# Optimization experiments

Hardware: AMD Instinct MI355X
Metric: run time of the kernel (lower is better)

## Reference

```python
import jax, jax.numpy as jnp
import numpy as np

B, T, C, H = 4, 2048, 768, 12
D = C // H  # head dim = 64
EPS = 1e-5


def setup_inputs() -> dict:
    key = jax.random.key(0)
    ks = jax.random.split(key, 12)
    s = lambda fan_in: 1.0 / np.sqrt(fan_in)
    return {
        "x": jax.random.normal(ks[0], (B, T, C), dtype=jnp.float32),
        "ln1_g": jnp.ones((C,), jnp.float32),
        "ln1_b": jnp.zeros((C,), jnp.float32),
        "w_attn": jax.random.normal(ks[1], (C, 3 * C), jnp.float32) * s(C),
        "b_attn": jnp.zeros((3 * C,), jnp.float32),
        "w_aproj": jax.random.normal(ks[2], (C, C), jnp.float32) * s(C),
        "b_aproj": jnp.zeros((C,), jnp.float32),
        "ln2_g": jnp.ones((C,), jnp.float32),
        "ln2_b": jnp.zeros((C,), jnp.float32),
        "w_fc": jax.random.normal(ks[3], (C, 4 * C), jnp.float32) * s(C),
        "b_fc": jnp.zeros((4 * C,), jnp.float32),
        "w_mproj": jax.random.normal(ks[4], (4 * C, C), jnp.float32) * s(4 * C),
        "b_mproj": jnp.zeros((C,), jnp.float32),
    }


def _layernorm(x, g, b):
    mu = jnp.mean(x, axis=-1, keepdims=True)
    var = jnp.mean(jnp.square(x - mu), axis=-1, keepdims=True)
    return (x - mu) * jax.lax.rsqrt(var + EPS) * g + b


def _attention(h, w_attn, b_attn, w_aproj, b_aproj):
    qkv = h @ w_attn + b_attn                          # [B,T,3C]
    q, k, v = jnp.split(qkv, 3, axis=-1)
    q = q.reshape(B, T, H, D)
    k = k.reshape(B, T, H, D)
    v = v.reshape(B, T, H, D)
    att = jnp.einsum("bqhd,bkhd->bhqk", q, k) * (1.0 / np.sqrt(D))
    causal = jnp.tril(jnp.ones((T, T), bool))
    att = jnp.where(causal, att, -jnp.inf)
    att = jax.nn.softmax(att, axis=-1)
    y = jnp.einsum("bhqk,bkhd->bqhd", att, v).reshape(B, T, C)
    return y @ w_aproj + b_aproj


def reference(x, ln1_g, ln1_b, w_attn, b_attn, w_aproj, b_aproj,
              ln2_g, ln2_b, w_fc, b_fc, w_mproj, b_mproj):
    x = x + _attention(_layernorm(x, ln1_g, ln1_b), w_attn, b_attn, w_aproj, b_aproj)
    h = _layernorm(x, ln2_g, ln2_b)
    h = jax.nn.gelu(h @ w_fc + b_fc, approximate=True)  # tanh approximation, matches F.gelu(approximate='tanh')
    x = x + (h @ w_mproj + b_mproj)
    return x
```

## Files before the change

### kernel.cpp

```cpp
#include <hip/hip_runtime.h>


typedef unsigned short ushortT;
typedef unsigned int uintT;
typedef __attribute__((ext_vector_type(8))) __bf16 bf16x8;
typedef __attribute__((ext_vector_type(4))) float f32x4;

#define MFMA16(a, b, c) __builtin_amdgcn_mfma_f32_16x16x32_bf16(a, b, c, 0, 0, 0)

__device__ inline float b2f(ushortT u) {
  return __uint_as_float(((uintT)u) << 16);
}
__device__ inline ushortT f2b(float f) {
  uintT x = __float_as_uint(f);
  uintT r = x + 0x7fffu + ((x >> 16) & 1u);
  return (ushortT)(r >> 16);
}
__device__ inline uintT pack_bf2(float a, float b) {
  return __builtin_amdgcn_perm(__float_as_uint(b), __float_as_uint(a),
                               0x07060302u);
}

__device__ inline float gelu_tanh(float v) {
  float t = 0.7978845608028654f * (v + 0.044715f * v * v * v);
  return v / (1.0f + __expf(-2.0f * t));
}

__device__ __forceinline__ void glds16(const ushortT* g, ushortT* l) {
  __builtin_amdgcn_global_load_lds(
      (const __attribute__((address_space(1))) unsigned int*)(const void*)g,
      (__attribute__((address_space(3))) unsigned int*)(void*)l, 16, 0, 0);
}

__global__ __launch_bounds__(256) void detect_dtype(
    const ushortT* __restrict__ w, int* __restrict__ flag) {
  __shared__ int red;
  if (threadIdx.x == 0) red = 0;
  __syncthreads();
  int crazy = 0;
  for (int i = threadIdx.x; i < 4096; i += 256) {
    uintT e = (w[2 * i] >> 7) & 0xFF;
    if (e >= 150) crazy = 1;
  }
  if (crazy) atomicOr(&red, 1);
  __syncthreads();
  if (threadIdx.x == 0) *flag = red;
}

struct VecArgs {
  const void* src[8];
  int n[8];
  int dstoff[8];
};
__global__ __launch_bounds__(256) void convert_vecs(
    VecArgs a, ushortT* __restrict__ pv, const int* __restrict__ flag) {
  int fl = *flag;
  int t = blockIdx.y;
  int i = blockIdx.x * 256 + threadIdx.x;
  if (i >= a.n[t]) return;
  float v = fl ? ((const float*)a.src[t])[i] : b2f(((const ushortT*)a.src[t])[i]);
  pv[a.dstoff[t] + i] = f2b(v);
}

__global__ __launch_bounds__(256) void transpose_any(
    const void* __restrict__ in, ushortT* __restrict__ out, int K, int N,
    const int* __restrict__ flag) {
  __shared__ ushortT t[32][33];
  int fl = *flag;
  int n0 = blockIdx.x * 32, k0 = blockIdx.y * 32;
  int x = threadIdx.x, y0 = threadIdx.y;
#pragma unroll
  for (int i = y0; i < 32; i += 8) {
    size_t idx = (size_t)(k0 + i) * N + n0 + x;
    t[i][x] = fl ? f2b(((const float*)in)[idx]) : ((const ushortT*)in)[idx];
  }
  __syncthreads();
#pragma unroll
  for (int i = y0; i < 32; i += 8)
    out[(size_t)(n0 + i) * K + k0 + x] = t[x][i];
}

__global__ __launch_bounds__(256) void vtrans_kernel(
    const ushortT* __restrict__ qkv, ushortT* __restrict__ vt) {
  const int T = 2048, C3 = 2304;
  __shared__ ushortT tile[64][65];
  int bh = blockIdx.y;
  int b = bh / 12, h = bh % 12;
  int t0 = blockIdx.x * 64;
  int col = threadIdx.x & 63, rowi = threadIdx.x >> 6;
#pragma unroll
  for (int rr = rowi; rr < 64; rr += 4)
    tile[rr][col] =
        qkv[((size_t)(b * T + t0 + rr)) * C3 + 1536 + h * 64 + col];
  __syncthreads();
#pragma unroll
  for (int dd = rowi; dd < 64; dd += 4)
    vt[((size_t)bh * 64 + dd) * T + t0 + col] = tile[col][dd];
}

template <int MODE>
__global__ __launch_bounds__(256) void ln_kernel(
    const void* __restrict__ xin, const ushortT* __restrict__ g,
    const ushortT* __restrict__ bb, ushortT* __restrict__ out,
    const int* __restrict__ flag) {
  const int C = 768;
  bool f32;
  if constexpr (MODE == 1) f32 = true; else f32 = (*flag != 0);
  size_t base = (size_t)blockIdx.x * C;
  int tid = threadIdx.x;
  const float* xf = (const float*)xin;
  const ushortT* xb = (const ushortT*)xin;
  float v0 = f32 ? xf[base + tid]       : b2f(xb[base + tid]);
  float v1 = f32 ? xf[base + tid + 256] : b2f(xb[base + tid + 256]);
  float v2 = f32 ? xf[base + tid + 512] : b2f(xb[base + tid + 512]);
  float s = v0 + v1 + v2;
  float q = v0 * v0 + v1 * v1 + v2 * v2;
#pragma unroll
  for (int off = 32; off; off >>= 1) {
    s += __shfl_xor(s, off);
    q += __shfl_xor(q, off);
  }
  __shared__ float as_[4], aq_[4];
  if ((tid & 63) == 0) { as_[tid >> 6] = s; aq_[tid >> 6] = q; }
  __syncthreads();
  s = as_[0] + as_[1] + as_[2] + as_[3];
  q = aq_[0] + aq_[1] + aq_[2] + aq_[3];
  float mu = s * (1.0f / 768.0f);
  float var = q * (1.0f / 768.0f) - mu * mu;
  float rs = rsqrtf(var + 1e-5f);
  ushortT* orow = out + base;
  orow[tid]       = f2b((v0 - mu) * rs * b2f(g[tid])       + b2f(bb[tid]));
  orow[tid + 256] = f2b((v1 - mu) * rs * b2f(g[tid + 256]) + b2f(bb[tid + 256]));
  orow[tid + 512] = f2b((v2 - mu) * rs * b2f(g[tid + 512]) + b2f(bb[tid + 512]));
}

template <int EPI, int MT, int BN, int NBN>
__global__ __launch_bounds__(256) void gemm_bf16(
    const ushortT* __restrict__ A, const ushortT* __restrict__ Bt,
    const ushortT* __restrict__ bias, const void* __restrict__ res,
    void* __restrict__ out, int N, int K, int nbm,
    const int* __restrict__ flag) {
  constexpr int MI = MT / 32, NI = BN / 32;
  __shared__ ushortT As[2 * MT * 32];
  __shared__ ushortT Bs[2 * BN * 32];
  int fl = (EPI >= 2) ? *flag : 0;
  int tid = threadIdx.x;
  int lane = tid & 63, wave = tid >> 6;
  int quad = lane >> 4, n = lane & 15;
  int wm = (wave >> 1) * (MT >> 1), wn = (wave & 1) * (BN >> 1);
  int l = blockIdx.x;
  int xcd = l & 7, j = l >> 3;
  int m0 = (xcd * (nbm >> 3) + j / NBN) * MT;
  int n0 = (j % NBN) * BN;

  int srow = lane >> 2, scol = (lane & 3) << 3;
  const ushortT* pa = A + (size_t)(m0 + wave * 16 + srow) * K + scol;
  const ushortT* pb = Bt + (size_t)(n0 + wave * 16 + srow) * K + scol;

  f32x4 acc[MI][NI] = {};

  for (int k0 = 0; k0 < K; k0 += 64) {
    __syncthreads();
#pragma unroll
    for (int i = 0; i < MT / 64; ++i) {
      glds16(pa + (size_t)i * 64 * K + k0, As + (wave * 16 + i * 64) * 32);
      glds16(pa + (size_t)i * 64 * K + k0 + 32,
             As + MT * 32 + (wave * 16 + i * 64) * 32);
    }
#pragma unroll
    for (int i = 0; i < BN / 64; ++i) {
      glds16(pb + (size_t)i * 64 * K + k0, Bs + (wave * 16 + i * 64) * 32);
      glds16(pb + (size_t)i * 64 * K + k0 + 32,
             Bs + BN * 32 + (wave * 16 + i * 64) * 32);
    }
    __syncthreads();
#pragma unroll
    for (int kk = 0; kk < 2; ++kk) {
      const ushortT* ap = As + kk * MT * 32;
      const ushortT* bp = Bs + kk * BN * 32;
      bf16x8 af[MI], bfr[NI];
#pragma unroll
      for (int mi = 0; mi < MI; ++mi)
        af[mi] = *(const bf16x8*)(ap + (wm + mi * 16 + n) * 32 + quad * 8);
#pragma unroll
      for (int ni = 0; ni < NI; ++ni)
        bfr[ni] = *(const bf16x8*)(bp + (wn + ni * 16 + n) * 32 + quad * 8);
#pragma unroll
      for (int mi = 0; mi < MI; ++mi)
#pragma unroll
        for (int ni = 0; ni < NI; ++ni)
          acc[mi][ni] = MFMA16(af[mi], bfr[ni], acc[mi][ni]);
    }
  }

#pragma unroll
  for (int mi = 0; mi < MI; ++mi) {
#pragma unroll
    for (int ni = 0; ni < NI; ++ni) {
      int gc = n0 + wn + ni * 16 + n;
      float bv = b2f(bias[gc]);
      int gr0 = m0 + wm + mi * 16 + quad * 4;
#pragma unroll
      for (int r = 0; r < 4; ++r) {
        size_t idx = (size_t)(gr0 + r) * N + gc;
        float v = acc[mi][ni][r] + bv;
        if constexpr (EPI == 1) v = gelu_tanh(v);
        if constexpr (EPI == 2) {
          v += fl ? ((const float*)res)[idx] : b2f(((const ushortT*)res)[idx]);
          ((float*)out)[idx] = v;
        } else if constexpr (EPI == 3) {
          v += ((const float*)res)[idx];
          if (fl) ((float*)out)[idx] = v;
          else    ((ushortT*)out)[idx] = f2b(v);
        } else {
          ((ushortT*)out)[idx] = f2b(v);
        }
      }
    }
  }
}

__global__ __launch_bounds__(256) void attn_kernel(
    const ushortT* __restrict__ qkv, const ushortT* __restrict__ vt,
    ushortT* __restrict__ y) {
  const int T = 2048, C3 = 2304;
  constexpr int LDK = 72, LDP = 72;
  __shared__ ushortT Ks[64 * LDK];
  __shared__ ushortT Vs[64 * LDK];
  __shared__ ushortT Ps[4 * 16 * LDP];
  int bh = blockIdx.y;
  int b = bh / 12, h = bh % 12;
  int pj = blockIdx.x;
  int tid = threadIdx.x;
  int lane = tid & 63, wave = tid >> 6;
  int quad = lane >> 4, n = lane & 15;

  const ushortT* base = qkv + (size_t)b * T * C3;
  const ushortT* kbase = base + 768 + h * 64;
  const ushortT* vbase = vt + (size_t)bh * 64 * T;
  ushortT* myP = Ps + wave * 16 * LDP;

  const float QS = 0.18033688011112042f;
  const float MB = 20.0f;

  int qtA = pj, qtB = 31 - pj;
  int nA = qtA + 1, ntot = 33;

  int trow = tid >> 3, tcol = (tid & 7) << 3;
  const ushortT* kg = kbase + (size_t)trow * C3 + tcol;
  const ushortT* vg = vbase + (size_t)trow * T + tcol;

  int qt = qtA;
  int qw = qt * 64 + wave * 16;
  bf16x8 aq[2];
  {
    const ushortT* qrow = base + (size_t)(qw + n) * C3 + h * 64 + quad * 8;
#pragma unroll
    for (int dh = 0; dh < 2; ++dh) {
      union { ushortT u[8]; bf16x8 v; } tmp;
#pragma unroll
      for (int j = 0; j < 8; ++j) tmp.u[j] = f2b(b2f(qrow[dh * 32 + j]) * QS);
      aq[dh] = tmp.v;
    }
  }
  f32x4 Ot[4] = {};
  float l_ = 0.f;

  uint4 kr0 = *(const uint4*)(kg);
  uint4 kr1 = *(const uint4*)(kg + (size_t)32 * C3);
  uint4 vr0 = *(const uint4*)(vg);
  uint4 vr1 = *(const uint4*)(vg + (size_t)32 * T);

  for (int t = 0; t < ntot; ++t) {
    int kt = (t < nA) ? t : t - nA;
    __syncthreads();
    *(uint4*)(Ks + trow * LDK + tcol) = kr0;
    *(uint4*)(Ks + (trow + 32) * LDK + tcol) = kr1;
    *(uint4*)(Vs + trow * LDK + tcol) = vr0;
    *(uint4*)(Vs + (trow + 32) * LDK + tcol) = vr1;
    __syncthreads();
    if (t + 1 < ntot) {
      int ktn = (t + 1 < nA) ? t + 1 : t + 1 - nA;
      int k0n = ktn << 6;
      kr0 = *(const uint4*)(kg + (size_t)k0n * C3);
      kr1 = *(const uint4*)(kg + (size_t)(k0n + 32) * C3);
      vr0 = *(const uint4*)(vg + k0n);
      vr1 = *(const uint4*)(vg + (size_t)32 * T + k0n);
    }

    f32x4 St[4];
#pragma unroll
    for (int g = 0; g < 4; ++g) {
      bf16x8 ka0 = *(const bf16x8*)(Ks + (g * 16 + n) * LDK + quad * 8);
      bf16x8 ka1 = *(const bf16x8*)(Ks + (g * 16 + n) * LDK + 32 + quad * 8);
      f32x4 z = {};
      z = MFMA16(ka0, aq[0], z);
      St[g] = MFMA16(ka1, aq[1], z);
    }
    if (kt == qt) {
      int lim = wave * 16 + n;
#pragma unroll
      for (int g = 0; g < 4; ++g)
#pragma unroll
        for (int r = 0; r < 4; ++r)
          if (g * 16 + quad * 4 + r > lim) St[g][r] = -1e30f;
    }
    float ls = 0.f;
#pragma unroll
    for (int g = 0; g < 4; ++g) {
      float p0 = exp2f(St[g][0] - MB);
      float p1 = exp2f(St[g][1] - MB);
      float p2 = exp2f(St[g][2] - MB);
      float p3 = exp2f(St[g][3] - MB);
      ls += (p0 + p1) + (p2 + p3);
      uint2 pk;
      pk.x = pack_bf2(p0, p1);
      pk.y = pack_bf2(p2, p3);
      *(uint2*)(myP + n * LDP + g * 16 + quad * 4) = pk;
    }
    ls += __shfl_xor(ls, 16);
    ls += __shfl_xor(ls, 32);
    l_ += ls;

    bf16x8 pb0 = *(const bf16x8*)(myP + n * LDP + quad * 8);
    bf16x8 pb1 = *(const bf16x8*)(myP + n * LDP + 32 + quad * 8);
#pragma unroll
    for (int dt = 0; dt < 4; ++dt) {
      bf16x8 va0 = *(const bf16x8*)(Vs + (dt * 16 + n) * LDK + quad * 8);
      bf16x8 va1 = *(const bf16x8*)(Vs + (dt * 16 + n) * LDK + 32 + quad * 8);
      Ot[dt] = MFMA16(va0, pb0, Ot[dt]);
      Ot[dt] = MFMA16(va1, pb1, Ot[dt]);
    }

    if (kt == qt) {
      float inv = 1.0f / l_;
      int qg = qw + n;
#pragma unroll
      for (int dt = 0; dt < 4; ++dt) {
        uint2 o;
        o.x = pack_bf2(Ot[dt][0] * inv, Ot[dt][1] * inv);
        o.y = pack_bf2(Ot[dt][2] * inv, Ot[dt][3] * inv);
        *(uint2*)(y + (size_t)(b * T + qg) * 768 + h * 64 + dt * 16 +
                  quad * 4) = o;
      }
      if (t + 1 < ntot) {
        qt = qtB;
        qw = qt * 64 + wave * 16;
        const ushortT* qrow =
            base + (size_t)(qw + n) * C3 + h * 64 + quad * 8;
#pragma unroll
        for (int dh = 0; dh < 2; ++dh) {
          union { ushortT u[8]; bf16x8 v; } tmp;
#pragma unroll
          for (int j = 0; j < 8; ++j)
            tmp.u[j] = f2b(b2f(qrow[dh * 32 + j]) * QS);
          aq[dh] = tmp.v;
        }
#pragma unroll
        for (int dt = 0; dt < 4; ++dt)
#pragma unroll
          for (int r = 0; r < 4; ++r) Ot[dt][r] = 0.f;
        l_ = 0.f;
      }
    }
  }
}

extern "C" void kernel_launch(void* const* d_in, const int* in_sizes, int n_in,
                              void* d_out, int out_size, void* d_ws,
                              size_t ws_size, hipStream_t stream) {
  (void)in_sizes; (void)n_in; (void)out_size; (void)ws_size;
  const void* x       = d_in[0];
  const void* w_attn  = d_in[3];
  const void* w_aproj = d_in[5];
  const void* w_fc    = d_in[9];
  const void* w_mproj = d_in[11];

  char* ws = (char*)d_ws;
  ushortT* h1  = (ushortT*)(ws);
  ushortT* qkv = (ushortT*)(ws + 12582912);
  ushortT* yb  = (ushortT*)(ws + 50331648);
  float*   x1  = (float*)(ws + 62914560);
  ushortT* fcg = (ushortT*)(ws + 88080384);
  ushortT* wT0 = (ushortT*)(ws + 138412032);
  ushortT* wT1 = (ushortT*)(ws + 141950976);
  ushortT* wT2 = (ushortT*)(ws + 143130624);
  ushortT* wT3 = (ushortT*)(ws + 147849216);
  ushortT* pv  = (ushortT*)(ws + 152567808);
  int*     flag = (int*)(ws + 152600576);
  ushortT* vt  = h1;
  ushortT* h2  = yb;

  const int O_LN1G = 0, O_LN1B = 768, O_BATT = 1536, O_BAPR = 3840,
            O_LN2G = 4608, O_LN2B = 5376, O_BFC = 6144, O_BMPR = 9216;

  detect_dtype<<<1, 256, 0, stream>>>((const ushortT*)w_fc, flag);

  VecArgs va;
  va.src[0] = d_in[1];  va.n[0] = 768;  va.dstoff[0] = O_LN1G;
  va.src[1] = d_in[2];  va.n[1] = 768;  va.dstoff[1] = O_LN1B;
  va.src[2] = d_in[4];  va.n[2] = 2304; va.dstoff[2] = O_BATT;
  va.src[3] = d_in[6];  va.n[3] = 768;  va.dstoff[3] = O_BAPR;
  va.src[4] = d_in[7];  va.n[4] = 768;  va.dstoff[4] = O_LN2G;
  va.src[5] = d_in[8];  va.n[5] = 768;  va.dstoff[5] = O_LN2B;
  va.src[6] = d_in[10]; va.n[6] = 3072; va.dstoff[6] = O_BFC;
  va.src[7] = d_in[12]; va.n[7] = 768;  va.dstoff[7] = O_BMPR;
  convert_vecs<<<dim3(12, 8), 256, 0, stream>>>(va, pv, flag);

  dim3 tb(32, 8);
  transpose_any<<<dim3(72, 24), tb, 0, stream>>>(w_attn, wT0, 768, 2304, flag);
  transpose_any<<<dim3(24, 24), tb, 0, stream>>>(w_aproj, wT1, 768, 768, flag);
  transpose_any<<<dim3(96, 24), tb, 0, stream>>>(w_fc, wT2, 768, 3072, flag);
  transpose_any<<<dim3(24, 96), tb, 0, stream>>>(w_mproj, wT3, 3072, 768, flag);

  ln_kernel<0><<<8192, 256, 0, stream>>>(x, pv + O_LN1G, pv + O_LN1B, h1, flag);
  gemm_bf16<0, 128, 128, 18><<<1152, 256, 0, stream>>>(
      h1, wT0, pv + O_BATT, nullptr, qkv, 2304, 768, 64, flag);
  vtrans_kernel<<<dim3(32, 48), 256, 0, stream>>>(qkv, vt);
  attn_kernel<<<dim3(16, 48), 256, 0, stream>>>(qkv, vt, yb);
  gemm_bf16<2, 64, 128, 6><<<768, 256, 0, stream>>>(
      yb, wT1, pv + O_BAPR, x, x1, 768, 768, 128, flag);
  ln_kernel<1><<<8192, 256, 0, stream>>>(x1, pv + O_LN2G, pv + O_LN2B, h2, flag);
  gemm_bf16<1, 128, 128, 24><<<1536, 256, 0, stream>>>(
      h2, wT2, pv + O_BFC, nullptr, fcg, 3072, 768, 64, flag);
  gemm_bf16<3, 64, 128, 6><<<768, 256, 0, stream>>>(
      fcg, wT3, pv + O_BMPR, x1, d_out, 768, 3072, 128, flag);
}
```

Baseline: 418.3 us.

## Replace GEMM with 128x256-tile, triple-buffered, 8-wave pipelined kernel

```diff
diff --git a/kernel.cpp b/kernel.cpp
--- a/kernel.cpp
+++ b/kernel.cpp
@@ -134,72 +134,127 @@
   orow[tid + 512] = f2b((v2 - mu) * rs * b2f(g[tid + 512]) + b2f(bb[tid + 512]));
 }
 
-template <int EPI, int MT, int BN, int NBN>
-__global__ __launch_bounds__(256) void gemm_bf16(
+template <int EPI>
+__global__ __launch_bounds__(512, 2) void gemm_dp(
     const ushortT* __restrict__ A, const ushortT* __restrict__ Bt,
     const ushortT* __restrict__ bias, const void* __restrict__ res,
-    void* __restrict__ out, int N, int K, int nbm,
+    void* __restrict__ out, int N, int K, int nbm, int nbn,
     const int* __restrict__ flag) {
-  constexpr int MI = MT / 32, NI = BN / 32;
-  __shared__ ushortT As[2 * MT * 32];
-  __shared__ ushortT Bs[2 * BN * 32];
+  __shared__ ushortT As3[3][128 * 64];
+  __shared__ ushortT Bs3[3][256 * 64];
   int fl = (EPI >= 2) ? *flag : 0;
   int tid = threadIdx.x;
   int lane = tid & 63, wave = tid >> 6;
-  int quad = lane >> 4, n = lane & 15;
-  int wm = (wave >> 1) * (MT >> 1), wn = (wave & 1) * (BN >> 1);
+  int quad = lane >> 4, n = lane & 15, n7 = n & 7;
+  int mg = wave >> 2, ng = wave & 3;
   int l = blockIdx.x;
   int xcd = l & 7, j = l >> 3;
-  int m0 = (xcd * (nbm >> 3) + j / NBN) * MT;
-  int n0 = (j % NBN) * BN;
-
-  int srow = lane >> 2, scol = (lane & 3) << 3;
-  const ushortT* pa = A + (size_t)(m0 + wave * 16 + srow) * K + scol;
-  const ushortT* pb = Bt + (size_t)(n0 + wave * 16 + srow) * K + scol;
-
-  f32x4 acc[MI][NI] = {};
-
-  for (int k0 = 0; k0 < K; k0 += 64) {
-    __syncthreads();
-#pragma unroll
-    for (int i = 0; i < MT / 64; ++i) {
-      glds16(pa + (size_t)i * 64 * K + k0, As + (wave * 16 + i * 64) * 32);
-      glds16(pa + (size_t)i * 64 * K + k0 + 32,
-             As + MT * 32 + (wave * 16 + i * 64) * 32);
-    }
-#pragma unroll
-    for (int i = 0; i < BN / 64; ++i) {
-      glds16(pb + (size_t)i * 64 * K + k0, Bs + (wave * 16 + i * 64) * 32);
-      glds16(pb + (size_t)i * 64 * K + k0 + 32,
-             Bs + BN * 32 + (wave * 16 + i * 64) * 32);
-    }
-    __syncthreads();
-#pragma unroll
-    for (int kk = 0; kk < 2; ++kk) {
-      const ushortT* ap = As + kk * MT * 32;
-      const ushortT* bp = Bs + kk * BN * 32;
-      bf16x8 af[MI], bfr[NI];
-#pragma unroll
-      for (int mi = 0; mi < MI; ++mi)
-        af[mi] = *(const bf16x8*)(ap + (wm + mi * 16 + n) * 32 + quad * 8);
-#pragma unroll
-      for (int ni = 0; ni < NI; ++ni)
-        bfr[ni] = *(const bf16x8*)(bp + (wn + ni * 16 + n) * 32 + quad * 8);
-#pragma unroll
-      for (int mi = 0; mi < MI; ++mi)
-#pragma unroll
-        for (int ni = 0; ni < NI; ++ni)
-          acc[mi][ni] = MFMA16(af[mi], bfr[ni], acc[mi][ni]);
-    }
-  }
-
-#pragma unroll
-  for (int mi = 0; mi < MI; ++mi) {
-#pragma unroll
-    for (int ni = 0; ni < NI; ++ni) {
-      int gc = n0 + wn + ni * 16 + n;
+  int m0 = (xcd * (nbm >> 3) + j / nbn) * 128;
+  int n0 = (j % nbn) * 256;
+
+  int trow = tid >> 3;
+  int tc = ((tid & 7) ^ (trow & 7)) << 3;
+  const ushortT* ga = A + (size_t)(m0 + trow) * K + tc;
+  const ushortT* gb = Bt + (size_t)(n0 + trow) * K + tc;
+  int lw = wave * 512;
+
+  const int c0 = (quad ^ n7) << 3;
+  const int c1 = ((4 + quad) ^ n7) << 3;
+  const int arow = (mg * 64 + n) * 64;
+  const int brow = (ng * 64 + n) * 64;
+
+  int kt = K >> 6;
+  f32x4 acc[4][4] = {};
+
+  auto stage_tile = [&](int tt, int slot) {
+    int kk0 = tt << 6;
+    ushortT* la = &As3[slot][0] + lw;
+    ushortT* lb = &Bs3[slot][0] + lw;
+    glds16(ga + kk0, la);
+    glds16(ga + (size_t)64 * K + kk0, la + 4096);
+    glds16(gb + kk0, lb);
+    glds16(gb + (size_t)64 * K + kk0, lb + 4096);
+    glds16(gb + (size_t)128 * K + kk0, lb + 8192);
+    glds16(gb + (size_t)192 * K + kk0, lb + 12288);
+  };
+
+  stage_tile(0, 0);
+  stage_tile(1, 1);
+  asm volatile("s_waitcnt vmcnt(6)" ::: "memory");
+  __builtin_amdgcn_s_barrier();
+
+  int cur = 0;
+  for (int t = 0; t < kt; ++t) {
+    const ushortT* ca = &As3[cur][0];
+    const ushortT* cb = &Bs3[cur][0];
+    int nxt = cur + 2; if (nxt >= 3) nxt -= 3;
+    bool pf = (t + 2) < kt;
+    int pk0 = (t + 2) << 6;
+    ushortT* la = &As3[nxt][0] + lw;
+    ushortT* lb = &Bs3[nxt][0] + lw;
+
+    bf16x8 af[4][2], bfr[2][2];
+#pragma unroll
+    for (int mi = 0; mi < 4; ++mi) {
+      af[mi][0] = *(const bf16x8*)(ca + arow + mi * 1024 + c0);
+      af[mi][1] = *(const bf16x8*)(ca + arow + mi * 1024 + c1);
+    }
+#pragma unroll
+    for (int ni = 0; ni < 2; ++ni) {
+      bfr[ni][0] = *(const bf16x8*)(cb + brow + ni * 1024 + c0);
+      bfr[ni][1] = *(const bf16x8*)(cb + brow + ni * 1024 + c1);
+    }
+    if (pf) {
+      glds16(ga + pk0, la);
+      glds16(ga + (size_t)64 * K + pk0, la + 4096);
+      glds16(gb + pk0, lb);
+    }
+    __builtin_amdgcn_s_barrier();
+    __builtin_amdgcn_s_setprio(1);
+#pragma unroll
+    for (int mi = 0; mi < 4; ++mi)
+#pragma unroll
+      for (int ni = 0; ni < 2; ++ni) {
+        acc[mi][ni] = MFMA16(af[mi][0], bfr[ni][0], acc[mi][ni]);
+        acc[mi][ni] = MFMA16(af[mi][1], bfr[ni][1], acc[mi][ni]);
+      }
+    __builtin_amdgcn_s_setprio(0);
+    __builtin_amdgcn_s_barrier();
+
+#pragma unroll
+    for (int ni = 0; ni < 2; ++ni) {
+      bfr[ni][0] = *(const bf16x8*)(cb + brow + (ni + 2) * 1024 + c0);
+      bfr[ni][1] = *(const bf16x8*)(cb + brow + (ni + 2) * 1024 + c1);
+    }
+    if (pf) {
+      glds16(gb + (size_t)64 * K + pk0, lb + 4096);
+      glds16(gb + (size_t)128 * K + pk0, lb + 8192);
+      glds16(gb + (size_t)192 * K + pk0, lb + 12288);
+    }
+    __builtin_amdgcn_s_barrier();
+    __builtin_amdgcn_s_setprio(1);
+#pragma unroll
+    for (int mi = 0; mi < 4; ++mi)
+#pragma unroll
+      for (int ni = 0; ni < 2; ++ni) {
+        acc[mi][ni + 2] = MFMA16(af[mi][0], bfr[ni][0], acc[mi][ni + 2]);
+        acc[mi][ni + 2] = MFMA16(af[mi][1], bfr[ni][1], acc[mi][ni + 2]);
+      }
+    __builtin_amdgcn_s_setprio(0);
+    if (pf) asm volatile("s_waitcnt vmcnt(6)" ::: "memory");
+    else    asm volatile("s_waitcnt vmcnt(0)" ::: "memory");
+    __builtin_amdgcn_s_barrier();
+
+    cur = cur + 1; if (cur == 3) cur = 0;
+  }
+
+#pragma unroll
+  for (int mi = 0; mi < 4; ++mi) {
+#pragma unroll
+    for (int ni = 0; ni < 4; ++ni) {
+      int gc = n0 + ng * 64 + ni * 16 + n;
       float bv = b2f(bias[gc]);
-      int gr0 = m0 + wm + mi * 16 + quad * 4;
+      int gr0 = m0 + mg * 64 + mi * 16 + quad * 4;
 #pragma unroll
       for (int r = 0; r < 4; ++r) {
         size_t idx = (size_t)(gr0 + r) * N + gc;
@@ -414,15 +469,15 @@
   transpose_any<<<dim3(24, 96), tb, 0, stream>>>(w_mproj, wT3, 3072, 768, flag);
 
   ln_kernel<0><<<8192, 256, 0, stream>>>(x, pv + O_LN1G, pv + O_LN1B, h1, flag);
-  gemm_bf16<0, 128, 128, 18><<<1152, 256, 0, stream>>>(
-      h1, wT0, pv + O_BATT, nullptr, qkv, 2304, 768, 64, flag);
+  gemm_dp<0><<<576, 512, 0, stream>>>(
+      h1, wT0, pv + O_BATT, nullptr, qkv, 2304, 768, 64, 9, flag);
   vtrans_kernel<<<dim3(32, 48), 256, 0, stream>>>(qkv, vt);
   attn_kernel<<<dim3(16, 48), 256, 0, stream>>>(qkv, vt, yb);
-  gemm_bf16<2, 64, 128, 6><<<768, 256, 0, stream>>>(
-      yb, wT1, pv + O_BAPR, x, x1, 768, 768, 128, flag);
+  gemm_dp<2><<<192, 512, 0, stream>>>(
+      yb, wT1, pv + O_BAPR, x, x1, 768, 768, 64, 3, flag);
   ln_kernel<1><<<8192, 256, 0, stream>>>(x1, pv + O_LN2G, pv + O_LN2B, h2, flag);
-  gemm_bf16<1, 128, 128, 24><<<1536, 256, 0, stream>>>(
-      h2, wT2, pv + O_BFC, nullptr, fcg, 3072, 768, 64, flag);
-  gemm_bf16<3, 64, 128, 6><<<768, 256, 0, stream>>>(
-      fcg, wT3, pv + O_BMPR, x1, d_out, 768, 3072, 128, flag);
-}
+  gemm_dp<1><<<768, 512, 0, stream>>>(
+      h2, wT2, pv + O_BFC, nullptr, fcg, 3072, 768, 64, 12, flag);
+  gemm_dp<3><<<192, 512, 0, stream>>>(
+      fcg, wT3, pv + O_BMPR, x1, d_out, 768, 3072, 64, 3, flag);
+}
```

Measured after the change: 419.3 us. No clear change (+0.2%).
